# Kernel tuning notes

Hardware: AMD Instinct MI355X
Metric: run time of the kernel (lower is better)

## Reference

```python
import jax, jax.numpy as jnp
import numpy as np

D_MODEL = 1024
D_OUT = 1024
N_EXPERTS = 8
TOP_K = 2


def setup_inputs() -> dict:
    key = jax.random.key(0)
    ks = jax.random.split(key, 5)
    b, t = 4, 4096
    inputs = jax.random.normal(ks[0], (b, t, D_MODEL), dtype=jnp.float32)
    # gate: Linear(input_dim, num_experts) -> weight (E, d), bias (E,)
    Wg = jax.random.normal(ks[1], (N_EXPERTS, D_MODEL), dtype=jnp.float32) / np.sqrt(D_MODEL)
    bg = jnp.zeros((N_EXPERTS,), dtype=jnp.float32)
    # experts: E x Linear(input_dim, output_dim) -> (E, d, f) and (E, f)
    We = jax.random.normal(ks[2], (N_EXPERTS, D_MODEL, D_OUT), dtype=jnp.float32) / np.sqrt(D_MODEL)
    be = jnp.zeros((N_EXPERTS, D_OUT), dtype=jnp.float32)
    return {"inputs": inputs, "Wg": Wg, "bg": bg, "We": We, "be": be}


def reference(inputs, Wg, bg, We, be):
    # gate logits: (b, t, E)
    gate_logits = jnp.einsum('btd,ed->bte', inputs, Wg) + bg
    # top-k per token (values descending, distinct indices) -> (b, t, k)
    topv, topi = jax.lax.top_k(gate_logits, TOP_K)
    gatew = jax.nn.sigmoid(topv).astype(inputs.dtype)            # (b, t, k)
    # scatter the k gate weights into a dense per-expert combine weight (b, t, E)
    onehot = jax.nn.one_hot(topi, N_EXPERTS, dtype=inputs.dtype)  # (b, t, k, E)
    combine = jnp.einsum('btk,btke->bte', gatew, onehot)          # (b, t, E)
    # per-expert linear outputs for all tokens: (b, t, E, f)
    expert_out = jnp.einsum('btd,edf->btef', inputs, We) + be
    # weighted combine over experts (unselected experts have weight 0)
    results = jnp.einsum('bte,btef->btf', combine, expert_out)
    return results
```

## Files before the change

### kernel.cpp

```cpp
#include <hip/hip_runtime.h>
#include <math.h>

#define DM 1024
#define DF 1024
#define NE 8
#define NBIN 16
#define MAXT 136
#define BM 128
#define BN 128
#define BKT 64

typedef __bf16 bf16x8 __attribute__((ext_vector_type(8)));
typedef __bf16 bf16x4 __attribute__((ext_vector_type(4)));
typedef float floatx4 __attribute__((ext_vector_type(4)));

typedef const __attribute__((address_space(1))) unsigned int* gas_t;
typedef __attribute__((address_space(3))) unsigned int* las_t;

__device__ __forceinline__ void ld_lds16(const void* g, void* l) {
    __builtin_amdgcn_global_load_lds((gas_t)g, (las_t)l, 16, 0, 0);
}


__global__ void convert_weT(const float* __restrict__ We, __bf16* __restrict__ WeT) {
    int n  = blockIdx.x * 256 + threadIdx.x;
    int kc = blockIdx.y * 8;
    int e  = blockIdx.z;
    const float* src = We + ((size_t)e << 20) + (size_t)kc * DF + n;
    bf16x8 v;
#pragma unroll
    for (int j = 0; j < 8; ++j) v[j] = (__bf16)src[(size_t)j * DF];
    *(bf16x8*)&WeT[((size_t)e << 20) + (size_t)n * DM + kc] = v;
}

__global__ void gate_kernel(const float4* __restrict__ X4, const float4* __restrict__ Wg4,
                            const float* __restrict__ bg, int* __restrict__ tok_e,
                            float* __restrict__ tok_w, __bf16* __restrict__ Xb, int T) {
    int wid  = threadIdx.x >> 6;
    int lane = threadIdx.x & 63;
    int t = blockIdx.x * 4 + wid;
    if (t >= T) return;
    float acc[NE] = {};
    float4 xs[4];
#pragma unroll
    for (int c = 0; c < 4; ++c) {
        float4 xv = X4[(size_t)t * 256 + c * 64 + lane];
        xs[c] = xv;
#pragma unroll
        for (int e = 0; e < NE; ++e) {
            float4 wv = Wg4[e * 256 + c * 64 + lane];
            acc[e] += xv.x * wv.x + xv.y * wv.y + xv.z * wv.z + xv.w * wv.w;
        }
    }
#pragma unroll
    for (int c = 0; c < 4; ++c) {
        bf16x4 v;
        v[0] = (__bf16)xs[c].x; v[1] = (__bf16)xs[c].y;
        v[2] = (__bf16)xs[c].z; v[3] = (__bf16)xs[c].w;
        *(bf16x4*)&Xb[(size_t)t * DM + c * 256 + lane * 4] = v;
    }
#pragma unroll
    for (int e = 0; e < NE; ++e) {
#pragma unroll
        for (int off = 32; off > 0; off >>= 1)
            acc[e] += __shfl_down(acc[e], off, 64);
    }
    if (lane == 0) {
        float l[NE];
#pragma unroll
        for (int e = 0; e < NE; ++e) l[e] = acc[e] + bg[e];
        int b0 = 0; float v0 = l[0];
        for (int e = 1; e < NE; ++e) if (l[e] > v0) { v0 = l[e]; b0 = e; }
        int b1 = -1; float v1 = -3.4e38f;
        for (int e = 0; e < NE; ++e) if (e != b0 && l[e] > v1) { v1 = l[e]; b1 = e; }
        tok_e[2 * t]     = b0;  tok_e[2 * t + 1] = b1;
        tok_w[2 * t]     = 1.f / (1.f + expf(-v0));
        tok_w[2 * t + 1] = 1.f / (1.f + expf(-v1));
    }
}

__global__ void hist_kernel(const int* __restrict__ tok_e, int* __restrict__ blk_cnt, int n) {
    int b = blockIdx.x, tid = threadIdx.x;
    int idx  = b * 256 + tid;
    int lane = tid & 63, w = tid >> 6;
    int bin = (idx < n) ? ((idx & 1) * NE + tok_e[idx]) : -1;
    __shared__ int wc[4][NBIN];
#pragma unroll
    for (int bx = 0; bx < NBIN; ++bx) {
        unsigned long long m = __ballot(bin == bx);
        if (lane == 0) wc[w][bx] = (int)__popcll(m);
    }
    __syncthreads();
    if (tid < NBIN) blk_cnt[b * NBIN + tid] = wc[0][tid] + wc[1][tid] + wc[2][tid] + wc[3][tid];
}

__global__ void scan_kernel(const int* __restrict__ blk_cnt, int* __restrict__ blk_base,
                            int4* __restrict__ wl, int* __restrict__ ntiles, int NB) {
    __shared__ int c[2048];
    __shared__ int tot[NBIN], base[NBIN];
    int tid = threadIdx.x;
    for (int i = tid; i < NB * NBIN; i += 256) c[i] = blk_cnt[i];
    __syncthreads();
    if (tid < NBIN) {
        int s = 0;
        for (int b = 0; b < NB; ++b) s += c[b * NBIN + tid];
        tot[tid] = s;
    }
    __syncthreads();
    if (tid == 0) {
        int s = 0;
        for (int b = 0; b < NBIN; ++b) { base[b] = s; s += tot[b]; }
    }
    __syncthreads();
    if (tid < NBIN) {
        int run = base[tid];
        for (int b = 0; b < NB; ++b) { int v = c[b * NBIN + tid]; c[b * NBIN + tid] = run; run += v; }
    }
    __syncthreads();
    for (int i = tid; i < NB * NBIN; i += 256) blk_base[i] = c[i];
    if (tid == 0) {
        for (int p = 0; p < 2; ++p) {
            int nt = 0;
            for (int e = 0; e < NE; ++e) {
                int bin = p * NE + e;
                int cnt = tot[bin], sg = base[bin];
                for (int r0 = 0; r0 < cnt; r0 += BM)
                    wl[p * MAXT + nt++] = make_int4(e, r0, sg, cnt);
            }
            ntiles[p] = nt;
        }
    }
}

__global__ void scatter_kernel(const int* __restrict__ tok_e, const float* __restrict__ tok_w,
                               const int* __restrict__ blk_base, int* __restrict__ gath_tok,
                               float* __restrict__ gath_w, int n) {
    int b = blockIdx.x, tid = threadIdx.x;
    int idx  = b * 256 + tid;
    int lane = tid & 63, w = tid >> 6;
    bool act = idx < n;
    int bin = act ? ((idx & 1) * NE + tok_e[idx]) : -1;
    __shared__ int wc[4][NBIN], wb[4][NBIN];
    int myrank = 0;
#pragma unroll
    for (int bx = 0; bx < NBIN; ++bx) {
        unsigned long long m = __ballot(bin == bx);
        if (lane == 0) wc[w][bx] = (int)__popcll(m);
        if (bin == bx) myrank = (int)__popcll(m & ((1ull << lane) - 1ull));
    }
    __syncthreads();
    if (tid < NBIN) {
        int run = blk_base[b * NBIN + tid];
#pragma unroll
        for (int wv = 0; wv < 4; ++wv) { wb[wv][tid] = run; run += wc[wv][tid]; }
    }
    __syncthreads();
    if (act) {
        int pos = wb[w][bin] + myrank;
        gath_tok[pos] = idx >> 1;
        gath_w[pos]   = tok_w[idx];
    }
}

template <bool ACC>
__global__ __launch_bounds__(256) void expert_gemm_mfma(
        const __bf16* __restrict__ Xb, const __bf16* __restrict__ WeT,
        const float* __restrict__ be, const int4* __restrict__ wl,
        const int* __restrict__ ntiles, const int* __restrict__ gtok,
        const float* __restrict__ gw, float* __restrict__ out) {
    if ((int)blockIdx.x >= ntiles[0]) return;
    int4 ent = wl[blockIdx.x];
    int e = ent.x, row0 = ent.y, seg = ent.z, n_e = ent.w;
    int col0 = blockIdx.y * BN;

    __shared__ __align__(16) __bf16 As0[BM * BKT];
    __shared__ __align__(16) __bf16 As1[BM * BKT];
    __shared__ __align__(16) __bf16 Bs0[BM * BKT];
    __shared__ __align__(16) __bf16 Bs1[BM * BKT];
    __shared__ int   s_tok[BM];
    __shared__ float s_w[BM];

    int tid = threadIdx.x;
    if (tid < BM) {
        int gr = row0 + tid;
        s_tok[tid] = (gr < n_e) ? gtok[seg + gr] : gtok[seg];
        s_w[tid]   = (gr < n_e) ? gw[seg + gr]   : 0.f;
    }
    __syncthreads();

    int lane = tid & 63, w = tid >> 6;
    int lr = lane >> 3;
    int kc = (lane & 7) ^ lr;

    const __bf16* aptr[4];
    const __bf16* bptr[4];
#pragma unroll
    for (int p = 0; p < 4; ++p) {
        int r = p * 32 + w * 8 + lr;
        aptr[p] = Xb + (size_t)s_tok[r] * DM + kc * 8;
        bptr[p] = WeT + ((size_t)e << 20) + (size_t)(col0 + r) * DM + kc * 8;
    }

    int wr = (w >> 1) * 64, wcc = (w & 1) * 64;
    int m16 = lane & 15, q = lane >> 4;
    int rsw = m16 & 7;

    floatx4 acc[4][4] = {};

    auto stage = [&](int koff, __bf16* AD, __bf16* BD) {
#pragma unroll
        for (int p = 0; p < 4; ++p) ld_lds16(aptr[p] + koff, &AD[(p * 4 + w) * 512]);
#pragma unroll
        for (int p = 0; p < 4; ++p) ld_lds16(bptr[p] + koff, &BD[(p * 4 + w) * 512]);
    };
    auto compute = [&](const __bf16* AS, const __bf16* BS) {
#pragma unroll
        for (int kt = 0; kt < 2; ++kt) {
            bf16x8 af[4], bfr[4];
#pragma unroll
            for (int i = 0; i < 4; ++i)
                af[i] = *(const bf16x8*)&AS[(wr + i * 16 + m16) * 64 + ((kt * 4 + q) ^ rsw) * 8];
#pragma unroll
            for (int i = 0; i < 4; ++i)
                bfr[i] = *(const bf16x8*)&BS[(wcc + i * 16 + m16) * 64 + ((kt * 4 + q) ^ rsw) * 8];
#pragma unroll
            for (int i = 0; i < 4; ++i)
#pragma unroll
                for (int j = 0; j < 4; ++j)
                    acc[i][j] = __builtin_amdgcn_mfma_f32_16x16x32_bf16(af[i], bfr[j], acc[i][j], 0, 0, 0);
        }
    };

    stage(0, As0, Bs0);
    __syncthreads();

    for (int k0 = 0; k0 < DM; k0 += 2 * BKT) {
        stage(k0 + BKT, As1, Bs1);
        compute(As0, Bs0);
        __syncthreads();
        if (k0 + 2 * BKT < DM) stage(k0 + 2 * BKT, As0, Bs0);
        compute(As1, Bs1);
        __syncthreads();
    }

#pragma unroll
    for (int j = 0; j < 4; ++j) {
        int c = col0 + wcc + j * 16 + m16;
        float bias = be[e * DF + c];
#pragma unroll
        for (int i = 0; i < 4; ++i) {
#pragma unroll
            for (int rg = 0; rg < 4; ++rg) {
                int rl = wr + i * 16 + q * 4 + rg;
                int gr = row0 + rl;
                if (gr < n_e) {
                    size_t o = (size_t)s_tok[rl] * DF + c;
                    float v = s_w[rl] * (acc[i][j][rg] + bias);
                    if (ACC) out[o] += v;
                    else     out[o] = v;
                }
            }
        }
    }
}

extern "C" void kernel_launch(void* const* d_in, const int* in_sizes, int n_in,
                              void* d_out, int out_size, void* d_ws, size_t ws_size,
                              hipStream_t stream) {
    const float* x  = (const float*)d_in[0];
    const float* Wg = (const float*)d_in[1];
    const float* bg = (const float*)d_in[2];
    const float* We = (const float*)d_in[3];
    const float* be = (const float*)d_in[4];
    float* out = (float*)d_out;

    int T = in_sizes[0] / DM;
    int n_slots = 2 * T;
    int NB = (n_slots + 255) / 256;

    char* ws = (char*)d_ws;
    size_t xb_bytes  = (size_t)T * DM * 2;
    size_t weT_bytes = (size_t)NE * DM * DF * 2;
    __bf16* Xb  = (__bf16*)ws;
    __bf16* WeT = (__bf16*)(ws + xb_bytes);
    char* rt = ws + xb_bytes + weT_bytes;
    int*   ntiles    = (int*)(rt + 0);
    int4*  wl        = (int4*)(rt + 64);
    int*   blk_cnt   = (int*)(rt + 64 + 2 * MAXT * 16);
    int*   blk_base  = (int*)((char*)blk_cnt + (size_t)NB * NBIN * 4);
    int*   tok_e     = (int*)((char*)blk_base + (size_t)NB * NBIN * 4);
    float* tok_w     = (float*)((char*)tok_e + (size_t)n_slots * 4);
    int*   gath_tok  = (int*)((char*)tok_w + (size_t)n_slots * 4);
    float* gath_w    = (float*)((char*)gath_tok + (size_t)n_slots * 4);

    convert_weT<<<dim3(DF / 256, DM / 8, NE), 256, 0, stream>>>(We, WeT);
    gate_kernel<<<(T + 3) / 4, 256, 0, stream>>>((const float4*)x, (const float4*)Wg,
                                                 bg, tok_e, tok_w, Xb, T);
    hist_kernel<<<NB, 256, 0, stream>>>(tok_e, blk_cnt, n_slots);
    scan_kernel<<<1, 256, 0, stream>>>(blk_cnt, blk_base, wl, ntiles, NB);
    scatter_kernel<<<NB, 256, 0, stream>>>(tok_e, tok_w, blk_base, gath_tok, gath_w, n_slots);

    dim3 grid(MAXT, DF / BN);
    expert_gemm_mfma<false><<<grid, 256, 0, stream>>>(Xb, WeT, be, wl, ntiles,
                                                      gath_tok, gath_w, out);
    expert_gemm_mfma<true><<<grid, 256, 0, stream>>>(Xb, WeT, be, wl + MAXT, ntiles + 1,
                                                     gath_tok, gath_w, out);
}
```

Measured before the change: 387.2 us.

## Stage GEMM epilogue through swizzled LDS for coalesced vector stores; remap block order

```diff
diff --git a/kernel.cpp b/kernel.cpp
--- a/kernel.cpp
+++ b/kernel.cpp
@@ -168,15 +168,18 @@
         const float* __restrict__ be, const int4* __restrict__ wl,
         const int* __restrict__ ntiles, const int* __restrict__ gtok,
         const float* __restrict__ gw, float* __restrict__ out) {
-    if ((int)blockIdx.x >= ntiles[0]) return;
-    int4 ent = wl[blockIdx.x];
+    int sw = (blockIdx.x & 7) * MAXT + (blockIdx.x >> 3);
+    int tix  = sw >> 3;
+    int col0 = (sw & 7) * BN;
+    if (tix >= ntiles[0]) return;
+    int4 ent = wl[tix];
     int e = ent.x, row0 = ent.y, seg = ent.z, n_e = ent.w;
-    int col0 = blockIdx.y * BN;
-
-    __shared__ __align__(16) __bf16 As0[BM * BKT];
-    __shared__ __align__(16) __bf16 As1[BM * BKT];
-    __shared__ __align__(16) __bf16 Bs0[BM * BKT];
-    __shared__ __align__(16) __bf16 Bs1[BM * BKT];
+
+    __shared__ __align__(16) char smem_raw[64 * 1024];
+    __bf16* As0 = (__bf16*)(smem_raw);
+    __bf16* As1 = (__bf16*)(smem_raw + 16384);
+    __bf16* Bs0 = (__bf16*)(smem_raw + 32768);
+    __bf16* Bs1 = (__bf16*)(smem_raw + 49152);
     __shared__ int   s_tok[BM];
     __shared__ float s_w[BM];
 
@@ -243,22 +246,46 @@
         __syncthreads();
     }
 
+    float* Cs = (float*)smem_raw;
 #pragma unroll
     for (int j = 0; j < 4; ++j) {
-        int c = col0 + wcc + j * 16 + m16;
-        float bias = be[e * DF + c];
 #pragma unroll
         for (int i = 0; i < 4; ++i) {
 #pragma unroll
             for (int rg = 0; rg < 4; ++rg) {
                 int rl = wr + i * 16 + q * 4 + rg;
-                int gr = row0 + rl;
-                if (gr < n_e) {
-                    size_t o = (size_t)s_tok[rl] * DF + c;
-                    float v = s_w[rl] * (acc[i][j][rg] + bias);
-                    if (ACC) out[o] += v;
-                    else     out[o] = v;
+                int cl = wcc + j * 16 + m16;
+                int quad = (cl >> 2) ^ (rl & 31);
+                Cs[rl * 128 + quad * 4 + (cl & 3)] = acc[i][j][rg];
+            }
+        }
+    }
+    __syncthreads();
+
+#pragma unroll
+    for (int rh = 0; rh < 2; ++rh) {
+        int rr = w * 32 + rh * 16 + (lane >> 2);
+        int gr2 = row0 + rr;
+        if (gr2 < n_e) {
+            int tok = s_tok[rr];
+            float wgt = s_w[rr];
+            float* orow = out + (size_t)tok * DF + col0;
+            const float* brow = be + e * DF + col0;
+#pragma unroll
+            for (int k = 0; k < 8; ++k) {
+                int cq = k * 4 + (lane & 3);
+                int c4 = cq * 4;
+                floatx4 v  = *(const floatx4*)&Cs[rr * 128 + ((cq ^ (rr & 31)) * 4)];
+                floatx4 bv = *(const floatx4*)&brow[c4];
+                floatx4 r;
+#pragma unroll
+                for (int z = 0; z < 4; ++z) r[z] = wgt * (v[z] + bv[z]);
+                if (ACC) {
+                    floatx4 o = *(const floatx4*)&orow[c4];
+#pragma unroll
+                    for (int z = 0; z < 4; ++z) r[z] += o[z];
                 }
+                *(floatx4*)&orow[c4] = r;
             }
         }
     }
@@ -300,9 +327,8 @@
     scan_kernel<<<1, 256, 0, stream>>>(blk_cnt, blk_base, wl, ntiles, NB);
     scatter_kernel<<<NB, 256, 0, stream>>>(tok_e, tok_w, blk_base, gath_tok, gath_w, n_slots);
 
-    dim3 grid(MAXT, DF / BN);
-    expert_gemm_mfma<false><<<grid, 256, 0, stream>>>(Xb, WeT, be, wl, ntiles,
-                                                      gath_tok, gath_w, out);
-    expert_gemm_mfma<true><<<grid, 256, 0, stream>>>(Xb, WeT, be, wl + MAXT, ntiles + 1,
-                                                     gath_tok, gath_w, out);
-}
+    expert_gemm_mfma<false><<<MAXT * 8, 256, 0, stream>>>(Xb, WeT, be, wl, ntiles,
+                                                          gath_tok, gath_w, out);
+    expert_gemm_mfma<true><<<MAXT * 8, 256, 0, stream>>>(Xb, WeT, be, wl + MAXT, ntiles + 1,
+                                                         gath_tok, gath_w, out);
+}
```

New measurement: 315.7 us. 1.23x faster.
